# Performance work log

Measured on AMD Instinct MI355X. Metric: run time of the kernel, lower is better.

Reference implementation:

```python
import jax, jax.numpy as jnp
import numpy as np

HEAD_DIM = 128
SCALE = 1.0 / np.sqrt(HEAD_DIM)  # standard 1/sqrt(d) attention scaling


def setup_inputs() -> dict:
    key = jax.random.key(0)
    kq, kk, kv = jax.random.split(key, 3)
    q = jax.random.normal(kq, (2, 32, 2048, HEAD_DIM), dtype=jnp.float16)
    k = jax.random.normal(kk, (2, 8, 2048, HEAD_DIM), dtype=jnp.float16)
    v = jax.random.normal(kv, (2, 8, 2048, HEAD_DIM), dtype=jnp.float16)
    return {"q": q, "k": k, "v": v}


def reference(q, k, v):
    # GQA attention: each of the g = H // KVH query heads in a group attends
    # against the group's single shared K/V head (no K/V duplication).
    b, h, sq, d = q.shape
    kvh = k.shape[1]
    g = h // kvh
    # [b, kvh, g, sq, d] -- group-packed Q, mirroring the kernel's _pack_q
    qg = q.reshape(b, kvh, g, sq, d)
    # fp32 accumulation as in flash-attention kernels
    scores = jnp.einsum(
        'bhgqd,bhkd->bhgqk',
        qg.astype(jnp.float32), k.astype(jnp.float32)) * SCALE
    p = jax.nn.softmax(scores, axis=-1)  # non-causal, full attention
    o = jnp.einsum('bhgqk,bhkd->bhgqd', p, v.astype(jnp.float32))
    return o.reshape(b, h, sq, d).astype(q.dtype)
```

## Files before the change

kernel.cpp:

```cpp
#include <hip/hip_runtime.h>
#include <hip/hip_bf16.h>

#define SEQ   2048
#define HD    128
#define BN    64
#define NITER (SEQ / BN)

typedef short bf16x8 __attribute__((ext_vector_type(8)));
typedef float f32x4  __attribute__((ext_vector_type(4)));

__device__ __forceinline__ unsigned pk2(float lo, float hi) {
  float2 t; t.x = lo; t.y = hi;
  __hip_bfloat162 r = __float22bfloat162_rn(t);
  union { __hip_bfloat162 h; unsigned u; } cv; cv.h = r;
  return cv.u;
}

__global__ __launch_bounds__(256, 2)
void fa_gqa_kernel(const float* __restrict__ Q,
                   const float* __restrict__ K,
                   const float* __restrict__ V,
                   float* __restrict__ O)
{
  __shared__ unsigned short kt_lds[64 * HD];
  __shared__ unsigned short vt_lds[HD * 64];
  __shared__ unsigned short p_lds[4][32 * BN];

  const int tid  = threadIdx.x;
  const int lane = tid & 63;
  const int w    = tid >> 6;
  const int c    = lane & 15;
  const int qh   = lane >> 4;

  const int F     = blockIdx.x;
  const int xcd   = F & 7;
  const int s     = F >> 3;
  const int bh    = xcd * 8 + (s >> 4);
  const int qtile = s & 15;

  const int b = bh >> 5;
  const int h = bh & 31;
  const long qrow0 = (long)bh * SEQ + qtile * 128 + w * 32;
  const float* Qw = Q + qrow0 * HD;
  float*       Ow = O + qrow0 * HD;
  const long kvoff = (long)(b * 8 + (h >> 2)) * SEQ * HD;
  const float* Kb = K + kvoff;
  const float* Vb = V + kvoff;

  bf16x8 qf[2][4];
#pragma unroll
  for (int qt = 0; qt < 2; ++qt)
#pragma unroll
    for (int dc = 0; dc < 4; ++dc) {
      const float4* qp = (const float4*)(Qw + (qt * 16 + c) * HD + dc * 32 + qh * 8);
      float4 a = qp[0], bq = qp[1];
      int4 t;
      t.x = (int)pk2(a.x, a.y);
      t.y = (int)pk2(a.z, a.w);
      t.z = (int)pk2(bq.x, bq.y);
      t.w = (int)pk2(bq.z, bq.w);
      qf[qt][dc] = *(bf16x8*)&t;
    }

  f32x4 oacc[2][8];
#pragma unroll
  for (int mt = 0; mt < 2; ++mt)
#pragma unroll
    for (int nt = 0; nt < 8; ++nt)
      oacc[mt][nt] = (f32x4){0.f, 0.f, 0.f, 0.f};

  float mst[2] = {-1e30f, -1e30f};
  float lst[2] = {0.f, 0.f};

  const float K1 = 0.08838834764831845f * 1.4426950408889634f;

  const int krow = tid >> 2;
  const int kq4  = tid & 3;
  const int rp   = tid >> 3;
  const int cc   = tid & 7;

  for (int it = 0; it < NITER; ++it) {
    const int k0 = it * BN;

    const float4* kp = (const float4*)(Kb + (long)(k0 + krow) * HD + kq4 * 32);
    float4 kf[8];
#pragma unroll
    for (int i = 0; i < 8; ++i) kf[i] = kp[i];

    const float* vp = Vb + (long)(k0 + 2 * rp) * HD + cc * 16;
    float4 xr[4], yr[4];
#pragma unroll
    for (int i = 0; i < 4; ++i) {
      xr[i] = ((const float4*)vp)[i];
      yr[i] = ((const float4*)(vp + HD))[i];
    }

    __syncthreads();

#pragma unroll
    for (int jj = 0; jj < 4; ++jj) {
      float4 e = kf[2 * jj], o = kf[2 * jj + 1];
      int4 wv;
      wv.x = (int)pk2(e.x, e.y);
      wv.y = (int)pk2(e.z, e.w);
      wv.z = (int)pk2(o.x, o.y);
      wv.w = (int)pk2(o.z, o.w);
      int j = kq4 * 4 + jj;
      int pos = j ^ (krow & 15);
      *(int4*)(kt_lds + krow * HD + pos * 8) = wv;
    }

    {
      unsigned* vt32 = (unsigned*)vt_lds;
      const int kk = 2 * rp;
      const float* xf = (const float*)xr;
      const float* yf = (const float*)yr;
#pragma unroll
      for (int d = 0; d < 16; ++d) {
        unsigned wv = pk2(xf[d], yf[d]);
        int dd = 16 * cc + d;
        int wi = dd * 32 + (((kk >> 3) ^ (dd & 7) ^ (dd >> 4)) << 2) + ((kk & 7) >> 1);
        vt32[wi] = wv;
      }
    }

    __syncthreads();

    f32x4 sacc[4][2];
#pragma unroll
    for (int kt = 0; kt < 4; ++kt)
#pragma unroll
      for (int qt = 0; qt < 2; ++qt)
        sacc[kt][qt] = (f32x4){0.f, 0.f, 0.f, 0.f};

#pragma unroll
    for (int dc = 0; dc < 4; ++dc) {
#pragma unroll
      for (int kt = 0; kt < 4; ++kt) {
        int row = kt * 16 + c;
        int pos = (4 * dc + qh) ^ c;
        bf16x8 af = *(const bf16x8*)(kt_lds + row * HD + pos * 8);
#pragma unroll
        for (int qt = 0; qt < 2; ++qt)
          sacc[kt][qt] = __builtin_amdgcn_mfma_f32_16x16x32_bf16(
              af, qf[qt][dc], sacc[kt][qt], 0, 0, 0);
      }
    }

    float alpha[2];
#pragma unroll
    for (int qt = 0; qt < 2; ++qt) {
      float mx = sacc[0][qt][0];
#pragma unroll
      for (int kt = 0; kt < 4; ++kt)
#pragma unroll
        for (int r = 0; r < 4; ++r)
          mx = fmaxf(mx, sacc[kt][qt][r]);
      mx = fmaxf(mx, __shfl_xor(mx, 16, 64));
      mx = fmaxf(mx, __shfl_xor(mx, 32, 64));
      float mnew = fmaxf(mst[qt], mx);
      alpha[qt] = __builtin_amdgcn_exp2f(K1 * (mst[qt] - mnew));
      mst[qt] = mnew;
      float nm = -K1 * mnew;
      float sum = 0.f;
#pragma unroll
      for (int kt = 0; kt < 4; ++kt)
#pragma unroll
        for (int r = 0; r < 4; ++r) {
          float p = __builtin_amdgcn_exp2f(fmaf(sacc[kt][qt][r], K1, nm));
          sacc[kt][qt][r] = p;
          sum += p;
        }
      lst[qt] = lst[qt] * alpha[qt] + sum;
    }

    unsigned short* pw = p_lds[w];
#pragma unroll
    for (int qt = 0; qt < 2; ++qt) {
      int qr = qt * 16 + c;
#pragma unroll
      for (int kt = 0; kt < 4; ++kt) {
        unsigned lo = pk2(sacc[kt][qt][0], sacc[kt][qt][1]);
        unsigned hi = pk2(sacc[kt][qt][2], sacc[kt][qt][3]);
        int kc8 = 2 * kt + (qh >> 1);
        int pos = kc8 ^ (qr & 7);
        *(uint2*)(pw + qr * BN + pos * 8 + (qh & 1) * 4) = make_uint2(lo, hi);
      }
    }

#pragma unroll
    for (int mt = 0; mt < 2; ++mt) {
#pragma unroll
      for (int r = 0; r < 4; ++r) {
        float av = __shfl(alpha[mt], 4 * qh + r, 64);
#pragma unroll
        for (int nt = 0; nt < 8; ++nt)
          oacc[mt][nt][r] *= av;
      }
    }

    __syncthreads();

#pragma unroll
    for (int kc = 0; kc < 2; ++kc) {
      bf16x8 pa[2];
#pragma unroll
      for (int mt = 0; mt < 2; ++mt) {
        int qr = mt * 16 + c;
        int pos = (4 * kc + qh) ^ (qr & 7);
        pa[mt] = *(const bf16x8*)(pw + qr * BN + pos * 8);
      }
#pragma unroll
      for (int nt = 0; nt < 8; ++nt) {
        int n = nt * 16 + c;
        int pos = (4 * kc + qh) ^ (n & 7) ^ (n >> 4);
        bf16x8 vb = *(const bf16x8*)(vt_lds + n * 64 + pos * 8);
#pragma unroll
        for (int mt = 0; mt < 2; ++mt)
          oacc[mt][nt] = __builtin_amdgcn_mfma_f32_16x16x32_bf16(
              pa[mt], vb, oacc[mt][nt], 0, 0, 0);
      }
    }
  }

  float linv[2];
#pragma unroll
  for (int qt = 0; qt < 2; ++qt) {
    float lf = lst[qt];
    lf += __shfl_xor(lf, 16, 64);
    lf += __shfl_xor(lf, 32, 64);
    linv[qt] = 1.0f / lf;
  }
#pragma unroll
  for (int mt = 0; mt < 2; ++mt) {
#pragma unroll
    for (int r = 0; r < 4; ++r) {
      float li = __shfl(linv[mt], 4 * qh + r, 64);
      float* orow = Ow + (mt * 16 + 4 * qh + r) * HD + c;
#pragma unroll
      for (int nt = 0; nt < 8; ++nt)
        orow[nt * 16] = oacc[mt][nt][r] * li;
    }
  }
}

extern "C" void kernel_launch(void* const* d_in, const int* in_sizes, int n_in,
                              void* d_out, int out_size, void* d_ws, size_t ws_size,
                              hipStream_t stream) {
  const float* q = (const float*)d_in[0];
  const float* k = (const float*)d_in[1];
  const float* v = (const float*)d_in[2];
  float* o = (float*)d_out;
  fa_gqa_kernel<<<dim3(1024), dim3(256), 0, stream>>>(q, k, v, o);
}
```

Measured before the change: 374.3 us.

## Keep P in registers via transposed PV MFMA, switch to fp16, raise occupancy

The kernel computes O transposed (V^T·P^T) using 16x16x16 f16 MFMA, so the softmax probabilities stay in registers in the S accumulator layout. This removes the per-wave P LDS buffer, its store/load round-trip and one __syncthreads per iteration. It also switches from bf16 to fp16 conversion (pkrtz), converts K/V before the barrier with a new V transpose layout, and raises the launch bound to 3 blocks per CU. The costs are twice as many smaller MFMAs, fp16 overflow risk with round-toward-zero, and register pressure from the higher occupancy target.

```diff
diff --git a/kernel.cpp b/kernel.cpp
--- a/kernel.cpp
+++ b/kernel.cpp
@@ -1,22 +1,21 @@
 #include <hip/hip_runtime.h>
-#include <hip/hip_bf16.h>
 
 #define SEQ   2048
 #define HD    128
 #define BN    64
 #define NITER (SEQ / BN)
 
-typedef short bf16x8 __attribute__((ext_vector_type(8)));
-typedef float f32x4  __attribute__((ext_vector_type(4)));
-
-__device__ __forceinline__ unsigned pk2(float lo, float hi) {
-  float2 t; t.x = lo; t.y = hi;
-  __hip_bfloat162 r = __float22bfloat162_rn(t);
-  union { __hip_bfloat162 h; unsigned u; } cv; cv.h = r;
-  return cv.u;
+typedef __fp16 f16x2 __attribute__((ext_vector_type(2)));
+typedef __fp16 f16x4 __attribute__((ext_vector_type(4)));
+typedef __fp16 f16x8 __attribute__((ext_vector_type(8)));
+typedef float  f32x4 __attribute__((ext_vector_type(4)));
+
+__device__ __forceinline__ unsigned pkh(float a, float b) {
+  auto h = __builtin_amdgcn_cvt_pkrtz(a, b);
+  return __builtin_bit_cast(unsigned, h);
 }
 
-__global__ __launch_bounds__(256, 2)
+__global__ __launch_bounds__(256, 3)
 void fa_gqa_kernel(const float* __restrict__ Q,
                    const float* __restrict__ K,
                    const float* __restrict__ V,
@@ -24,7 +23,6 @@
 {
   __shared__ unsigned short kt_lds[64 * HD];
   __shared__ unsigned short vt_lds[HD * 64];
-  __shared__ unsigned short p_lds[4][32 * BN];
 
   const int tid  = threadIdx.x;
   const int lane = tid & 63;
@@ -47,7 +45,7 @@
   const float* Kb = K + kvoff;
   const float* Vb = V + kvoff;
 
-  bf16x8 qf[2][4];
+  f16x8 qf[2][4];
 #pragma unroll
   for (int qt = 0; qt < 2; ++qt)
 #pragma unroll
@@ -55,19 +53,19 @@
       const float4* qp = (const float4*)(Qw + (qt * 16 + c) * HD + dc * 32 + qh * 8);
       float4 a = qp[0], bq = qp[1];
       int4 t;
-      t.x = (int)pk2(a.x, a.y);
-      t.y = (int)pk2(a.z, a.w);
-      t.z = (int)pk2(bq.x, bq.y);
-      t.w = (int)pk2(bq.z, bq.w);
-      qf[qt][dc] = *(bf16x8*)&t;
+      t.x = (int)pkh(a.x, a.y);
+      t.y = (int)pkh(a.z, a.w);
+      t.z = (int)pkh(bq.x, bq.y);
+      t.w = (int)pkh(bq.z, bq.w);
+      qf[qt][dc] = __builtin_bit_cast(f16x8, t);
     }
 
   f32x4 oacc[2][8];
 #pragma unroll
   for (int mt = 0; mt < 2; ++mt)
 #pragma unroll
-    for (int nt = 0; nt < 8; ++nt)
-      oacc[mt][nt] = (f32x4){0.f, 0.f, 0.f, 0.f};
+    for (int dt = 0; dt < 8; ++dt)
+      oacc[mt][dt] = (f32x4){0.f, 0.f, 0.f, 0.f};
 
   float mst[2] = {-1e30f, -1e30f};
   float lst[2] = {0.f, 0.f};
@@ -76,52 +74,56 @@
 
   const int krow = tid >> 2;
   const int kq4  = tid & 3;
-  const int rp   = tid >> 3;
-  const int cc   = tid & 7;
+  const int kq   = tid >> 4;
+  const int dc8  = tid & 15;
 
   for (int it = 0; it < NITER; ++it) {
     const int k0 = it * BN;
 
-    const float4* kp = (const float4*)(Kb + (long)(k0 + krow) * HD + kq4 * 32);
-    float4 kf[8];
-#pragma unroll
-    for (int i = 0; i < 8; ++i) kf[i] = kp[i];
-
-    const float* vp = Vb + (long)(k0 + 2 * rp) * HD + cc * 16;
-    float4 xr[4], yr[4];
-#pragma unroll
-    for (int i = 0; i < 4; ++i) {
-      xr[i] = ((const float4*)vp)[i];
-      yr[i] = ((const float4*)(vp + HD))[i];
+    const float* kp = Kb + (long)(k0 + krow) * HD + kq4 * 32;
+    int4 ks[4];
+#pragma unroll
+    for (int jj = 0; jj < 4; ++jj) {
+      float4 e = ((const float4*)kp)[2 * jj];
+      float4 o = ((const float4*)kp)[2 * jj + 1];
+      ks[jj].x = (int)pkh(e.x, e.y);
+      ks[jj].y = (int)pkh(e.z, e.w);
+      ks[jj].z = (int)pkh(o.x, o.y);
+      ks[jj].w = (int)pkh(o.z, o.w);
+    }
+
+    const float* vp = Vb + (long)(k0 + 4 * kq) * HD + dc8 * 8;
+    float4 vr[4][2];
+#pragma unroll
+    for (int r = 0; r < 4; ++r) {
+      vr[r][0] = ((const float4*)(vp + r * HD))[0];
+      vr[r][1] = ((const float4*)(vp + r * HD))[1];
+    }
+    uint2 vs[8];
+#pragma unroll
+    for (int jd = 0; jd < 8; ++jd) {
+      const int hsel = jd >> 2, e = jd & 3;
+      float x0 = ((const float*)&vr[0][hsel])[e];
+      float x1 = ((const float*)&vr[1][hsel])[e];
+      float x2 = ((const float*)&vr[2][hsel])[e];
+      float x3 = ((const float*)&vr[3][hsel])[e];
+      vs[jd].x = pkh(x0, x1);
+      vs[jd].y = pkh(x2, x3);
     }
 
     __syncthreads();
 
 #pragma unroll
     for (int jj = 0; jj < 4; ++jj) {
-      float4 e = kf[2 * jj], o = kf[2 * jj + 1];
-      int4 wv;
-      wv.x = (int)pk2(e.x, e.y);
-      wv.y = (int)pk2(e.z, e.w);
-      wv.z = (int)pk2(o.x, o.y);
-      wv.w = (int)pk2(o.z, o.w);
       int j = kq4 * 4 + jj;
       int pos = j ^ (krow & 15);
-      *(int4*)(kt_lds + krow * HD + pos * 8) = wv;
-    }
-
-    {
-      unsigned* vt32 = (unsigned*)vt_lds;
-      const int kk = 2 * rp;
-      const float* xf = (const float*)xr;
-      const float* yf = (const float*)yr;
-#pragma unroll
-      for (int d = 0; d < 16; ++d) {
-        unsigned wv = pk2(xf[d], yf[d]);
-        int dd = 16 * cc + d;
-        int wi = dd * 32 + (((kk >> 3) ^ (dd & 7) ^ (dd >> 4)) << 2) + ((kk & 7) >> 1);
-        vt32[wi] = wv;
-      }
+      *(int4*)(kt_lds + krow * HD + pos * 8) = ks[jj];
+    }
+#pragma unroll
+    for (int jd = 0; jd < 8; ++jd) {
+      int d = dc8 * 8 + jd;
+      int pos = kq ^ (d & 15) ^ (d >> 4);
+      *(uint2*)(vt_lds + d * 64 + pos * 4) = vs[jd];
     }
 
     __syncthreads();
@@ -139,10 +141,10 @@
       for (int kt = 0; kt < 4; ++kt) {
         int row = kt * 16 + c;
         int pos = (4 * dc + qh) ^ c;
-        bf16x8 af = *(const bf16x8*)(kt_lds + row * HD + pos * 8);
+        f16x8 af = *(const f16x8*)(kt_lds + row * HD + pos * 8);
 #pragma unroll
         for (int qt = 0; qt < 2; ++qt)
-          sacc[kt][qt] = __builtin_amdgcn_mfma_f32_16x16x32_bf16(
+          sacc[kt][qt] = __builtin_amdgcn_mfma_f32_16x16x32_f16(
               af, qf[qt][dc], sacc[kt][qt], 0, 0, 0);
       }
     }
@@ -174,51 +176,33 @@
       lst[qt] = lst[qt] * alpha[qt] + sum;
     }
 
-    unsigned short* pw = p_lds[w];
-#pragma unroll
-    for (int qt = 0; qt < 2; ++qt) {
-      int qr = qt * 16 + c;
-#pragma unroll
-      for (int kt = 0; kt < 4; ++kt) {
-        unsigned lo = pk2(sacc[kt][qt][0], sacc[kt][qt][1]);
-        unsigned hi = pk2(sacc[kt][qt][2], sacc[kt][qt][3]);
-        int kc8 = 2 * kt + (qh >> 1);
-        int pos = kc8 ^ (qr & 7);
-        *(uint2*)(pw + qr * BN + pos * 8 + (qh & 1) * 4) = make_uint2(lo, hi);
+    f16x4 pf[4][2];
+#pragma unroll
+    for (int kt = 0; kt < 4; ++kt)
+#pragma unroll
+      for (int qt = 0; qt < 2; ++qt) {
+        uint2 u;
+        u.x = pkh(sacc[kt][qt][0], sacc[kt][qt][1]);
+        u.y = pkh(sacc[kt][qt][2], sacc[kt][qt][3]);
+        pf[kt][qt] = __builtin_bit_cast(f16x4, u);
       }
-    }
-
-#pragma unroll
-    for (int mt = 0; mt < 2; ++mt) {
-#pragma unroll
-      for (int r = 0; r < 4; ++r) {
-        float av = __shfl(alpha[mt], 4 * qh + r, 64);
-#pragma unroll
-        for (int nt = 0; nt < 8; ++nt)
-          oacc[mt][nt][r] *= av;
-      }
-    }
-
-    __syncthreads();
-
-#pragma unroll
-    for (int kc = 0; kc < 2; ++kc) {
-      bf16x8 pa[2];
-#pragma unroll
-      for (int mt = 0; mt < 2; ++mt) {
-        int qr = mt * 16 + c;
-        int pos = (4 * kc + qh) ^ (qr & 7);
-        pa[mt] = *(const bf16x8*)(pw + qr * BN + pos * 8);
-      }
-#pragma unroll
-      for (int nt = 0; nt < 8; ++nt) {
-        int n = nt * 16 + c;
-        int pos = (4 * kc + qh) ^ (n & 7) ^ (n >> 4);
-        bf16x8 vb = *(const bf16x8*)(vt_lds + n * 64 + pos * 8);
-#pragma unroll
-        for (int mt = 0; mt < 2; ++mt)
-          oacc[mt][nt] = __builtin_amdgcn_mfma_f32_16x16x32_bf16(
-              pa[mt], vb, oacc[mt][nt], 0, 0, 0);
+
+#pragma unroll
+    for (int mt = 0; mt < 2; ++mt)
+#pragma unroll
+      for (int dt = 0; dt < 8; ++dt)
+        oacc[mt][dt] *= alpha[mt];
+
+#pragma unroll
+    for (int kt = 0; kt < 4; ++kt) {
+#pragma unroll
+      for (int dt = 0; dt < 8; ++dt) {
+        int pos = (4 * kt + qh) ^ c ^ dt;
+        f16x4 vf = *(const f16x4*)(vt_lds + (dt * 16 + c) * 64 + pos * 4);
+#pragma unroll
+        for (int qt = 0; qt < 2; ++qt)
+          oacc[qt][dt] = __builtin_amdgcn_mfma_f32_16x16x16f16(
+              vf, pf[kt][qt], oacc[qt][dt], 0, 0, 0);
       }
     }
   }
@@ -234,12 +218,9 @@
 #pragma unroll
   for (int mt = 0; mt < 2; ++mt) {
 #pragma unroll
-    for (int r = 0; r < 4; ++r) {
-      float li = __shfl(linv[mt], 4 * qh + r, 64);
-      float* orow = Ow + (mt * 16 + 4 * qh + r) * HD + c;
-#pragma unroll
-      for (int nt = 0; nt < 8; ++nt)
-        orow[nt * 16] = oacc[mt][nt][r] * li;
+    for (int dt = 0; dt < 8; ++dt) {
+      f32x4 ov = oacc[mt][dt] * linv[mt];
+      *(f32x4*)(Ow + (mt * 16 + c) * HD + dt * 16 + qh * 4) = ov;
     }
   }
 }
```

New measurement: 808.3 us. 116% more time.
